# Kernel optimization log

Measured on AMD Instinct MI355X. Metric: run time of the kernel, lower is better.

Reference implementation:

```python
import jax, jax.numpy as jnp
import numpy as np
from jax.scipy.linalg import expm

N_QUBITS = 13
N_LAYERS = 4  # ceil(log2(13))


def _apply_2axes(T, M, a0, a1):
    """Apply 4x4 matrix M to the pair of 2-dim axes (a0, a1) of tensor T."""
    nd = T.ndim
    T = jnp.moveaxis(T, (a0, a1), (nd - 2, nd - 1))
    s = T.shape
    T = (T.reshape(s[:-2] + (4,)) @ M.T).reshape(s)
    return jnp.moveaxis(T, (nd - 2, nd - 1), (a0, a1))


def _conv_pairs(n):
    pairs = [(2 * i, 2 * i + 1) for i in range(n // 2)]
    if n > 2:
        pairs += [(2 * i + 1, (2 * i + 2) % n) for i in range(n // 2)]
    return pairs


def _conv_state(psi, U, n):
    # psi: [B] + [2]*n pure state
    for q0, q1 in _conv_pairs(n):
        psi = _apply_2axes(psi, U, 1 + q0, 1 + q1)
    return psi


def _conv_dm(rho, U, n):
    # rho: [B] + [2]*n (rows) + [2]*n (cols); apply U on rows, U* on cols
    Uc = U.conj()
    for q0, q1 in _conv_pairs(n):
        rho = _apply_2axes(rho, U, 1 + q0, 1 + q1)
        rho = _apply_2axes(rho, Uc, 1 + n + q0, 1 + n + q1)
    return rho


def _pool_dm(rho, n):
    # measure-and-discard qubits 0..n//2-1 (with index shifting these are the
    # original even-indexed qubits); averaging over outcomes == partial trace.
    measured = [2 * i for i in range(n // 2)]
    cur = n
    for q in reversed(measured):  # descending so lower indices stay valid
        rho = jnp.trace(rho, axis1=1 + q, axis2=1 + cur + q)
        cur -= 1
    return rho, cur


def setup_inputs() -> dict:
    key = jax.random.key(0)
    k1, k2, k3, k4 = jax.random.split(key, 4)
    B, D = 2, 2 ** N_QUBITS
    return {
        "psi_real": jax.random.normal(k1, (B, D), dtype=jnp.float32),
        "psi_imag": jax.random.normal(k2, (B, D), dtype=jnp.float32),
        "H_real": jax.random.normal(k3, (N_LAYERS, 4, 4), dtype=jnp.float32),
        "H_imag": jax.random.normal(k4, (N_LAYERS, 4, 4), dtype=jnp.float32),
    }


def reference(psi_real, psi_imag, H_real, H_imag):
    B = psi_real.shape[0]
    n = N_QUBITS
    psi = (psi_real + 1j * psi_imag).astype(jnp.complex64)
    psi = psi / jnp.linalg.norm(psi, axis=1, keepdims=True)
    H = (H_real + 1j * H_imag).astype(jnp.complex64)
    # anti-hermitian generator -> unitary gate per layer
    Us = [expm(H[i] - H[i].conj().T) for i in range(N_LAYERS)]

    # layer 0: conv on pure state, then convert to density matrix, then pool
    psi = psi.reshape((B,) + (2,) * n)
    psi = _conv_state(psi, Us[0], n)
    flat = psi.reshape(B, -1)
    rho = (flat[:, :, None] * flat[:, None, :].conj()).reshape((B,) + (2,) * (2 * n))
    rho, n = _pool_dm(rho, n)

    for i in range(1, N_LAYERS):
        rho = _conv_dm(rho, Us[i], n)
        rho, n = _pool_dm(rho, n)

    # n == 1 here: measure qubit 0, return P(outcome 0)
    rho = rho.reshape(B, 2, 2)
    return rho[:, 0, 0].real
```

## Files before the change

kernel.cpp:

```cpp
#include <hip/hip_runtime.h>


#define NT 512
#define DIM 8192

__device__ __forceinline__ float2 cadd(float2 a, float2 b) {
    return make_float2(a.x + b.x, a.y + b.y);
}
__device__ __forceinline__ float2 cmac(float2 acc, float2 a, float2 b) {
    acc.x = fmaf(a.x, b.x, fmaf(-a.y, b.y, acc.x));
    acc.y = fmaf(a.x, b.y, fmaf(a.y, b.x, acc.y));
    return acc;
}
__device__ __forceinline__ float2 shflc(float2 v, int src) {
    return make_float2(__shfl(v.x, src, 64), __shfl(v.y, src, 64));
}
__device__ __forceinline__ float2 cmac2(float2 acc, float2 u, float2 us, float2 a) {
    acc.x = fmaf(a.x, u.x, acc.x);
    acc.y = fmaf(a.x, u.y, acc.y);
    acc.x = fmaf(a.y, us.x, acc.x);
    acc.y = fmaf(a.y, us.y, acc.y);
    return acc;
}

__device__ float2 expm_entry(const float* __restrict__ Hr,
                             const float* __restrict__ Hi) {
    const int lane = threadIdx.x & 63;
    const int m = lane >> 4, e = lane & 15, r = e >> 2, c = e & 3;
    const int base = lane & 48;

    float are = Hr[m * 16 + r * 4 + c] - Hr[m * 16 + c * 4 + r];
    float aim = Hi[m * 16 + r * 4 + c] + Hi[m * 16 + c * 4 + r];

    float v = fabsf(are) + fabsf(aim);
    v += __shfl_xor(v, 1, 64);
    v += __shfl_xor(v, 2, 64);
    v = fmaxf(v, __shfl_xor(v, 4, 64));
    v = fmaxf(v, __shfl_xor(v, 8, 64));
    v = fmaxf(v, __shfl_xor(v, 16, 64));
    v = fmaxf(v, __shfl_xor(v, 32, 64));

    int s = 0;
    while (v > 0.25f && s < 30) { v *= 0.5f; s++; }
    const float scale = ldexpf(1.0f, -s);

    float2 X = make_float2(are * scale, aim * scale);
    float2 E = X;
    if (r == c) E.x += 1.0f;
    float2 T = X;
    for (int k = 2; k <= 10; k++) {
        float2 acc = make_float2(0.f, 0.f);
        #pragma unroll
        for (int kk = 0; kk < 4; kk++) {
            float2 t = shflc(T, base + r * 4 + kk);
            float2 x = shflc(X, base + kk * 4 + c);
            acc = cmac(acc, t, x);
        }
        const float inv = 1.0f / (float)k;
        T = make_float2(acc.x * inv, acc.y * inv);
        E = cadd(E, T);
    }
    for (int i = 0; i < s; i++) {
        float2 acc = make_float2(0.f, 0.f);
        #pragma unroll
        for (int kk = 0; kk < 4; kk++) {
            float2 a = shflc(E, base + r * 4 + kk);
            float2 bb = shflc(E, base + kk * 4 + c);
            acc = cmac(acc, a, bb);
        }
        E = acc;
    }
    return E;
}

__device__ __forceinline__ void loadU(float2 E, int L, float2* u, float2* us) {
    #pragma unroll
    for (int e = 0; e < 16; e++) {
        u[e] = shflc(E, (L << 4) | e);
        us[e] = make_float2(-u[e].y, u[e].x);
    }
}

__device__ __forceinline__ int swz(int e) {
    return e ^ ((e >> 4) & 15) ^ ((e >> 8) & 3);
}

template<int MASK>
__device__ __forceinline__ int deposit(int t) {
    int r = 0;
    #pragma unroll
    for (int bpos = 0; bpos < 13; bpos++) {
        if (MASK & (1 << bpos)) { r |= (t & 1) << bpos; t >>= 1; }
    }
    return r;
}

template<int B3, int B2, int B1, int B0>
__device__ __forceinline__ int eaddr(int base, int i) {
    return base | (((i >> 3) & 1) << B3) | (((i >> 2) & 1) << B2)
                | (((i >> 1) & 1) << B1) | ((i & 1) << B0);
}

template<int B3, int B2, int B1, int B0, int MASK>
__device__ __forceinline__ void phase_read(float2* v, const float2* psi, int t) {
    const int base = deposit<MASK>(t);
    #pragma unroll
    for (int i = 0; i < 16; i++) v[i] = psi[swz(eaddr<B3, B2, B1, B0>(base, i))];
}
template<int B3, int B2, int B1, int B0, int MASK>
__device__ __forceinline__ void phase_write(const float2* v, float2* psi, int t) {
    const int base = deposit<MASK>(t);
    #pragma unroll
    for (int i = 0; i < 16; i++) psi[swz(eaddr<B3, B2, B1, B0>(base, i))] = v[i];
}

template<int KA, int KB>
__device__ __forceinline__ void apply_gate(float2* v, const float2* u, const float2* us) {
    const int MA = 1 << KA, MB = 1 << KB;
    #pragma unroll
    for (int i = 0; i < 16; i++) {
        if (i & (MA | MB)) continue;
        float2 a0 = v[i], a1 = v[i | MB], a2 = v[i | MA], a3 = v[i | MA | MB];
        float2 n0 = make_float2(0.f, 0.f);
        n0 = cmac2(n0, u[0], us[0], a0);  n0 = cmac2(n0, u[1], us[1], a1);
        n0 = cmac2(n0, u[2], us[2], a2);  n0 = cmac2(n0, u[3], us[3], a3);
        float2 n1 = make_float2(0.f, 0.f);
        n1 = cmac2(n1, u[4], us[4], a0);  n1 = cmac2(n1, u[5], us[5], a1);
        n1 = cmac2(n1, u[6], us[6], a2);  n1 = cmac2(n1, u[7], us[7], a3);
        float2 n2 = make_float2(0.f, 0.f);
        n2 = cmac2(n2, u[8], us[8], a0);  n2 = cmac2(n2, u[9], us[9], a1);
        n2 = cmac2(n2, u[10], us[10], a2); n2 = cmac2(n2, u[11], us[11], a3);
        float2 n3 = make_float2(0.f, 0.f);
        n3 = cmac2(n3, u[12], us[12], a0); n3 = cmac2(n3, u[13], us[13], a1);
        n3 = cmac2(n3, u[14], us[14], a2); n3 = cmac2(n3, u[15], us[15], a3);
        v[i] = n0; v[i | MB] = n1; v[i | MA] = n2; v[i | MA | MB] = n3;
    }
}

__global__ __launch_bounds__(NT) void qcnn_kernel(
    const float* __restrict__ pr, const float* __restrict__ pi,
    const float* __restrict__ Hr, const float* __restrict__ Hi,
    float* __restrict__ out) {
    __shared__ float2 psi[DIM];
    const int tid = threadIdx.x;
    const int b = blockIdx.x;

    const float* prb = pr + b * DIM;
    const float* pib = pi + b * DIM;
    float re[16], im[16];
    #pragma unroll
    for (int i = 0; i < 16; i++) {
        re[i] = prb[tid | (i << 9)];
        im[i] = pib[tid | (i << 9)];
    }

    float2 E = expm_entry(Hr, Hi);

    float2 v[16];
    float norm2p = 0.f;
    #pragma unroll
    for (int i = 0; i < 16; i++) {
        v[i] = make_float2(re[i], im[i]);
        norm2p = fmaf(re[i], re[i], fmaf(im[i], im[i], norm2p));
    }

    float2 u[16], us[16];
    loadU(E, 0, u, us);

    apply_gate<3, 2>(v, u, us);
    apply_gate<1, 0>(v, u, us);
    apply_gate<2, 1>(v, u, us);
    phase_write<12, 11, 10, 9, 0x01FF>(v, psi, tid);
    __syncthreads();

    phase_read<8, 7, 6, 5, 0x1E1F>(v, psi, tid);
    apply_gate<3, 2>(v, u, us);
    apply_gate<1, 0>(v, u, us);
    apply_gate<2, 1>(v, u, us);
    phase_write<8, 7, 6, 5, 0x1E1F>(v, psi, tid);
    __syncthreads();

    phase_read<3, 2, 1, 0, 0x1FF0>(v, psi, tid);
    apply_gate<2, 1>(v, u, us);
    apply_gate<1, 0>(v, u, us);
    phase_write<3, 2, 1, 0, 0x1FF0>(v, psi, tid);
    __syncthreads();

    phase_read<5, 4, 3, 2, 0x1FC3>(v, psi, tid);
    apply_gate<2, 1>(v, u, us);
    apply_gate<3, 2>(v, u, us);
    apply_gate<1, 0>(v, u, us);
    phase_write<5, 4, 3, 2, 0x1FC3>(v, psi, tid);
    __syncthreads();

    phase_read<11, 9, 8, 7, 0x147F>(v, psi, tid);
    apply_gate<2, 1>(v, u, us);
    loadU(E, 1, u, us);
    apply_gate<3, 2>(v, u, us);
    phase_write<11, 9, 8, 7, 0x147F>(v, psi, tid);
    __syncthreads();

    phase_read<7, 5, 3, 1, 0x1F55>(v, psi, tid);
    apply_gate<3, 2>(v, u, us);
    apply_gate<1, 0>(v, u, us);
    apply_gate<2, 1>(v, u, us);
    phase_write<7, 5, 3, 1, 0x1F55>(v, psi, tid);
    __syncthreads();

    phase_read<9, 7, 1, 0, 0x1D7C>(v, psi, tid);
    apply_gate<3, 2>(v, u, us);
    apply_gate<1, 0>(v, u, us);
    loadU(E, 2, u, us);
    apply_gate<1, 0>(v, u, us);
    phase_write<9, 7, 1, 0, 0x1D7C>(v, psi, tid);
    __syncthreads();

    phase_read<9, 5, 1, 0, 0x1DDC>(v, psi, tid);
    apply_gate<3, 2>(v, u, us);
    apply_gate<2, 1>(v, u, us);
    apply_gate<0, 3>(v, u, us);
    loadU(E, 3, u, us);
    apply_gate<2, 0>(v, u, us);

    float s0 = 0.f;
    #pragma unroll
    for (int i = 0; i < 16; i += 2) {
        s0 = fmaf(v[i].x, v[i].x, fmaf(v[i].y, v[i].y, s0));
    }

    #pragma unroll
    for (int off = 1; off < 64; off <<= 1) {
        s0 += __shfl_xor(s0, off, 64);
        norm2p += __shfl_xor(norm2p, off, 64);
    }
    __syncthreads();
    if ((tid & 63) == 0) psi[tid >> 6] = make_float2(s0, norm2p);
    __syncthreads();
    if (tid == 0) {
        float S = 0.f, Nrm = 0.f;
        #pragma unroll
        for (int w = 0; w < NT / 64; w++) { S += psi[w].x; Nrm += psi[w].y; }
        out[b] = S / Nrm;
    }
}

extern "C" void kernel_launch(void* const* d_in, const int* in_sizes, int n_in,
                              void* d_out, int out_size, void* d_ws, size_t ws_size,
                              hipStream_t stream) {
    const float* pr = (const float*)d_in[0];
    const float* pi = (const float*)d_in[1];
    const float* Hr = (const float*)d_in[2];
    const float* Hi = (const float*)d_in[3];
    float* out = (float*)d_out;
    qcnn_kernel<<<dim3(out_size), dim3(NT), 0, stream>>>(pr, pi, Hr, Hi, out);
}
```

Measured before the change: 81.50 us.

## Use 32 amplitudes per thread with 5-qubit phases to cut LDS round trips

Halves the block to 256 threads so each thread holds 32 amplitudes covering 5 qubits, and redesigns the gate schedule so fewer shared-memory exchange phases and barriers are needed (six instead of seven). The complex multiply-accumulate is rewritten on 2-wide vector types to encourage packed FP32 FMA instructions, and the LDS swizzle is changed to match the new access patterns. The cost is higher register pressure (64 floats of state plus the gate matrices) and fewer threads for latency hiding.

```diff
diff --git a/kernel.cpp b/kernel.cpp
--- a/kernel.cpp
+++ b/kernel.cpp
@@ -1,13 +1,15 @@
 #include <hip/hip_runtime.h>
 
 
-#define NT 512
+#define NT 256
 #define DIM 8192
 
-__device__ __forceinline__ float2 cadd(float2 a, float2 b) {
+typedef float v2f __attribute__((ext_vector_type(2)));
+
+__device__ __forceinline__ float2 cadds(float2 a, float2 b) {
     return make_float2(a.x + b.x, a.y + b.y);
 }
-__device__ __forceinline__ float2 cmac(float2 acc, float2 a, float2 b) {
+__device__ __forceinline__ float2 cmacs(float2 acc, float2 a, float2 b) {
     acc.x = fmaf(a.x, b.x, fmaf(-a.y, b.y, acc.x));
     acc.y = fmaf(a.x, b.y, fmaf(a.y, b.x, acc.y));
     return acc;
@@ -15,22 +17,20 @@
 __device__ __forceinline__ float2 shflc(float2 v, int src) {
     return make_float2(__shfl(v.x, src, 64), __shfl(v.y, src, 64));
 }
-__device__ __forceinline__ float2 cmac2(float2 acc, float2 u, float2 us, float2 a) {
-    acc.x = fmaf(a.x, u.x, acc.x);
-    acc.y = fmaf(a.x, u.y, acc.y);
-    acc.x = fmaf(a.y, us.x, acc.x);
-    acc.y = fmaf(a.y, us.y, acc.y);
+
+__device__ __forceinline__ v2f cma(v2f acc, v2f u, v2f us, v2f a) {
+#pragma clang fp contract(fast)
+    v2f ax = __builtin_shufflevector(a, a, 0, 0);
+    v2f ay = __builtin_shufflevector(a, a, 1, 1);
+    acc = ax * u + acc;
+    acc = ay * us + acc;
     return acc;
 }
 
-__device__ float2 expm_entry(const float* __restrict__ Hr,
-                             const float* __restrict__ Hi) {
+__device__ float2 expm_compute(float are, float aim) {
     const int lane = threadIdx.x & 63;
-    const int m = lane >> 4, e = lane & 15, r = e >> 2, c = e & 3;
+    const int e = lane & 15, r = e >> 2, c = e & 3;
     const int base = lane & 48;
-
-    float are = Hr[m * 16 + r * 4 + c] - Hr[m * 16 + c * 4 + r];
-    float aim = Hi[m * 16 + r * 4 + c] + Hi[m * 16 + c * 4 + r];
 
     float v = fabsf(are) + fabsf(aim);
     v += __shfl_xor(v, 1, 64);
@@ -54,11 +54,11 @@
         for (int kk = 0; kk < 4; kk++) {
             float2 t = shflc(T, base + r * 4 + kk);
             float2 x = shflc(X, base + kk * 4 + c);
-            acc = cmac(acc, t, x);
+            acc = cmacs(acc, t, x);
         }
         const float inv = 1.0f / (float)k;
         T = make_float2(acc.x * inv, acc.y * inv);
-        E = cadd(E, T);
+        E = cadds(E, T);
     }
     for (int i = 0; i < s; i++) {
         float2 acc = make_float2(0.f, 0.f);
@@ -66,157 +66,152 @@
         for (int kk = 0; kk < 4; kk++) {
             float2 a = shflc(E, base + r * 4 + kk);
             float2 bb = shflc(E, base + kk * 4 + c);
-            acc = cmac(acc, a, bb);
+            acc = cmacs(acc, a, bb);
         }
         E = acc;
     }
     return E;
 }
 
-__device__ __forceinline__ void loadU(float2 E, int L, float2* u, float2* us) {
-    #pragma unroll
-    for (int e = 0; e < 16; e++) {
-        u[e] = shflc(E, (L << 4) | e);
-        us[e] = make_float2(-u[e].y, u[e].x);
+__device__ __forceinline__ void loadU(float2 E, int L, v2f* u, v2f* us) {
+    #pragma unroll
+    for (int k = 0; k < 16; k++) {
+        float ur = __shfl(E.x, (L << 4) | k, 64);
+        float ui = __shfl(E.y, (L << 4) | k, 64);
+        u[k] = (v2f){ur, ui};
+        us[k] = (v2f){-ui, ur};
     }
 }
 
 __device__ __forceinline__ int swz(int e) {
-    return e ^ ((e >> 4) & 15) ^ ((e >> 8) & 3);
+    return e ^ ((e >> 3) & 14) ^ ((e >> 7) & 15) ^ ((e >> 10) & 14);
 }
 
 template<int MASK>
 __device__ __forceinline__ int deposit(int t) {
     int r = 0;
     #pragma unroll
-    for (int bpos = 0; bpos < 13; bpos++) {
-        if (MASK & (1 << bpos)) { r |= (t & 1) << bpos; t >>= 1; }
+    for (int p = 0; p < 13; p++) {
+        if (MASK & (1 << p)) { r |= (t & 1) << p; t >>= 1; }
     }
     return r;
 }
 
-template<int B3, int B2, int B1, int B0>
-__device__ __forceinline__ int eaddr(int base, int i) {
-    return base | (((i >> 3) & 1) << B3) | (((i >> 2) & 1) << B2)
-                | (((i >> 1) & 1) << B1) | ((i & 1) << B0);
-}
-
-template<int B3, int B2, int B1, int B0, int MASK>
-__device__ __forceinline__ void phase_read(float2* v, const float2* psi, int t) {
+template<int B4, int B3, int B2, int B1, int B0>
+__device__ __forceinline__ int eaddr5(int base, int i) {
+    return base | (((i >> 4) & 1) << B4) | (((i >> 3) & 1) << B3)
+                | (((i >> 2) & 1) << B2) | (((i >> 1) & 1) << B1)
+                | ((i & 1) << B0);
+}
+
+template<int B4, int B3, int B2, int B1, int B0, int MASK>
+__device__ __forceinline__ void phase_read(v2f* v, const v2f* psi, int t) {
     const int base = deposit<MASK>(t);
     #pragma unroll
-    for (int i = 0; i < 16; i++) v[i] = psi[swz(eaddr<B3, B2, B1, B0>(base, i))];
-}
-template<int B3, int B2, int B1, int B0, int MASK>
-__device__ __forceinline__ void phase_write(const float2* v, float2* psi, int t) {
+    for (int i = 0; i < 32; i++) v[i] = psi[swz(eaddr5<B4, B3, B2, B1, B0>(base, i))];
+}
+template<int B4, int B3, int B2, int B1, int B0, int MASK>
+__device__ __forceinline__ void phase_write(const v2f* v, v2f* psi, int t) {
     const int base = deposit<MASK>(t);
     #pragma unroll
-    for (int i = 0; i < 16; i++) psi[swz(eaddr<B3, B2, B1, B0>(base, i))] = v[i];
+    for (int i = 0; i < 32; i++) psi[swz(eaddr5<B4, B3, B2, B1, B0>(base, i))] = v[i];
 }
 
 template<int KA, int KB>
-__device__ __forceinline__ void apply_gate(float2* v, const float2* u, const float2* us) {
+__device__ __forceinline__ void apply_gate(v2f* v, const v2f* u, const v2f* us) {
     const int MA = 1 << KA, MB = 1 << KB;
     #pragma unroll
-    for (int i = 0; i < 16; i++) {
+    for (int i = 0; i < 32; i++) {
         if (i & (MA | MB)) continue;
-        float2 a0 = v[i], a1 = v[i | MB], a2 = v[i | MA], a3 = v[i | MA | MB];
-        float2 n0 = make_float2(0.f, 0.f);
-        n0 = cmac2(n0, u[0], us[0], a0);  n0 = cmac2(n0, u[1], us[1], a1);
-        n0 = cmac2(n0, u[2], us[2], a2);  n0 = cmac2(n0, u[3], us[3], a3);
-        float2 n1 = make_float2(0.f, 0.f);
-        n1 = cmac2(n1, u[4], us[4], a0);  n1 = cmac2(n1, u[5], us[5], a1);
-        n1 = cmac2(n1, u[6], us[6], a2);  n1 = cmac2(n1, u[7], us[7], a3);
-        float2 n2 = make_float2(0.f, 0.f);
-        n2 = cmac2(n2, u[8], us[8], a0);  n2 = cmac2(n2, u[9], us[9], a1);
-        n2 = cmac2(n2, u[10], us[10], a2); n2 = cmac2(n2, u[11], us[11], a3);
-        float2 n3 = make_float2(0.f, 0.f);
-        n3 = cmac2(n3, u[12], us[12], a0); n3 = cmac2(n3, u[13], us[13], a1);
-        n3 = cmac2(n3, u[14], us[14], a2); n3 = cmac2(n3, u[15], us[15], a3);
+        v2f a0 = v[i], a1 = v[i | MB], a2 = v[i | MA], a3 = v[i | MA | MB];
+        v2f z = {0.f, 0.f};
+        v2f n0 = cma(cma(cma(cma(z, u[0], us[0], a0), u[1], us[1], a1),
+                         u[2], us[2], a2), u[3], us[3], a3);
+        v2f n1 = cma(cma(cma(cma(z, u[4], us[4], a0), u[5], us[5], a1),
+                         u[6], us[6], a2), u[7], us[7], a3);
+        v2f n2 = cma(cma(cma(cma(z, u[8], us[8], a0), u[9], us[9], a1),
+                         u[10], us[10], a2), u[11], us[11], a3);
+        v2f n3 = cma(cma(cma(cma(z, u[12], us[12], a0), u[13], us[13], a1),
+                         u[14], us[14], a2), u[15], us[15], a3);
         v[i] = n0; v[i | MB] = n1; v[i | MA] = n2; v[i | MA | MB] = n3;
     }
 }
 
-__global__ __launch_bounds__(NT) void qcnn_kernel(
+__global__ __launch_bounds__(NT, 1) void qcnn_kernel(
     const float* __restrict__ pr, const float* __restrict__ pi,
     const float* __restrict__ Hr, const float* __restrict__ Hi,
     float* __restrict__ out) {
-    __shared__ float2 psi[DIM];
-    const int tid = threadIdx.x;
+    __shared__ v2f psi[DIM];
+    const int t = threadIdx.x;
     const int b = blockIdx.x;
+    const int lane = t & 63;
+    const int m = lane >> 4, ee = lane & 15, r = ee >> 2, c = ee & 3;
+
+    float hra = Hr[m * 16 + r * 4 + c], hrb = Hr[m * 16 + c * 4 + r];
+    float hia = Hi[m * 16 + r * 4 + c], hib = Hi[m * 16 + c * 4 + r];
 
     const float* prb = pr + b * DIM;
     const float* pib = pi + b * DIM;
-    float re[16], im[16];
-    #pragma unroll
-    for (int i = 0; i < 16; i++) {
-        re[i] = prb[tid | (i << 9)];
-        im[i] = pib[tid | (i << 9)];
-    }
-
-    float2 E = expm_entry(Hr, Hi);
-
-    float2 v[16];
-    float norm2p = 0.f;
-    #pragma unroll
-    for (int i = 0; i < 16; i++) {
-        v[i] = make_float2(re[i], im[i]);
-        norm2p = fmaf(re[i], re[i], fmaf(im[i], im[i], norm2p));
-    }
-
-    float2 u[16], us[16];
+    v2f v[32];
+    #pragma unroll
+    for (int i = 0; i < 32; i++)
+        v[i] = (v2f){prb[t | (i << 8)], pib[t | (i << 8)]};
+
+    float2 E = expm_compute(hra - hrb, hia + hib);
+
+    float norm2 = 0.f;
+    #pragma unroll
+    for (int i = 0; i < 32; i++)
+        norm2 = fmaf(v[i].x, v[i].x, fmaf(v[i].y, v[i].y, norm2));
+
+    v2f u[16], us[16];
     loadU(E, 0, u, us);
 
-    apply_gate<3, 2>(v, u, us);
-    apply_gate<1, 0>(v, u, us);
-    apply_gate<2, 1>(v, u, us);
-    phase_write<12, 11, 10, 9, 0x01FF>(v, psi, tid);
-    __syncthreads();
-
-    phase_read<8, 7, 6, 5, 0x1E1F>(v, psi, tid);
-    apply_gate<3, 2>(v, u, us);
-    apply_gate<1, 0>(v, u, us);
-    apply_gate<2, 1>(v, u, us);
-    phase_write<8, 7, 6, 5, 0x1E1F>(v, psi, tid);
-    __syncthreads();
-
-    phase_read<3, 2, 1, 0, 0x1FF0>(v, psi, tid);
-    apply_gate<2, 1>(v, u, us);
-    apply_gate<1, 0>(v, u, us);
-    phase_write<3, 2, 1, 0, 0x1FF0>(v, psi, tid);
-    __syncthreads();
-
-    phase_read<5, 4, 3, 2, 0x1FC3>(v, psi, tid);
-    apply_gate<2, 1>(v, u, us);
-    apply_gate<3, 2>(v, u, us);
-    apply_gate<1, 0>(v, u, us);
-    phase_write<5, 4, 3, 2, 0x1FC3>(v, psi, tid);
-    __syncthreads();
-
-    phase_read<11, 9, 8, 7, 0x147F>(v, psi, tid);
-    apply_gate<2, 1>(v, u, us);
+    apply_gate<4, 3>(v, u, us);
+    apply_gate<2, 1>(v, u, us);
+    apply_gate<3, 2>(v, u, us);
+    phase_write<12, 11, 10, 9, 8, 0x00FF>(v, psi, t);
+    __syncthreads();
+
+    phase_read<8, 7, 6, 5, 4, 0x1E0F>(v, psi, t);
+    apply_gate<4, 3>(v, u, us);
+    apply_gate<2, 1>(v, u, us);
+    apply_gate<3, 2>(v, u, us);
+    phase_write<8, 7, 6, 5, 4, 0x1E0F>(v, psi, t);
+    __syncthreads();
+
+    phase_read<4, 3, 2, 1, 0, 0x1FE0>(v, psi, t);
+    apply_gate<4, 3>(v, u, us);
+    apply_gate<2, 1>(v, u, us);
+    apply_gate<3, 2>(v, u, us);
+    apply_gate<1, 0>(v, u, us);
     loadU(E, 1, u, us);
-    apply_gate<3, 2>(v, u, us);
-    phase_write<11, 9, 8, 7, 0x147F>(v, psi, tid);
-    __syncthreads();
-
-    phase_read<7, 5, 3, 1, 0x1F55>(v, psi, tid);
-    apply_gate<3, 2>(v, u, us);
-    apply_gate<1, 0>(v, u, us);
-    apply_gate<2, 1>(v, u, us);
-    phase_write<7, 5, 3, 1, 0x1F55>(v, psi, tid);
-    __syncthreads();
-
-    phase_read<9, 7, 1, 0, 0x1D7C>(v, psi, tid);
-    apply_gate<3, 2>(v, u, us);
+    apply_gate<3, 1>(v, u, us);
     apply_gate<1, 0>(v, u, us);
     loadU(E, 2, u, us);
     apply_gate<1, 0>(v, u, us);
-    phase_write<9, 7, 1, 0, 0x1D7C>(v, psi, tid);
-    __syncthreads();
-
-    phase_read<9, 5, 1, 0, 0x1DDC>(v, psi, tid);
-    apply_gate<3, 2>(v, u, us);
+    phase_write<4, 3, 2, 1, 0, 0x1FE0>(v, psi, t);
+    __syncthreads();
+
+    phase_read<9, 8, 7, 5, 4, 0x1C4F>(v, psi, t);
+    loadU(E, 0, u, us);
+    apply_gate<4, 3>(v, u, us);
+    apply_gate<1, 0>(v, u, us);
+    loadU(E, 1, u, us);
+    apply_gate<2, 1>(v, u, us);
+    phase_write<9, 8, 7, 5, 4, 0x1C4F>(v, psi, t);
+    __syncthreads();
+
+    phase_read<11, 9, 7, 5, 3, 0x1557>(v, psi, t);
+    apply_gate<4, 3>(v, u, us);
+    apply_gate<3, 2>(v, u, us);
+    apply_gate<1, 0>(v, u, us);
+    loadU(E, 2, u, us);
+    apply_gate<3, 1>(v, u, us);
+    phase_write<11, 9, 7, 5, 3, 0x1557>(v, psi, t);
+    __syncthreads();
+
+    phase_read<12, 9, 5, 1, 0, 0x0DDC>(v, psi, t);
     apply_gate<2, 1>(v, u, us);
     apply_gate<0, 3>(v, u, us);
     loadU(E, 3, u, us);
@@ -224,19 +219,18 @@
 
     float s0 = 0.f;
     #pragma unroll
-    for (int i = 0; i < 16; i += 2) {
+    for (int i = 0; i < 32; i += 2)
         s0 = fmaf(v[i].x, v[i].x, fmaf(v[i].y, v[i].y, s0));
-    }
 
     #pragma unroll
     for (int off = 1; off < 64; off <<= 1) {
         s0 += __shfl_xor(s0, off, 64);
-        norm2p += __shfl_xor(norm2p, off, 64);
-    }
-    __syncthreads();
-    if ((tid & 63) == 0) psi[tid >> 6] = make_float2(s0, norm2p);
-    __syncthreads();
-    if (tid == 0) {
+        norm2 += __shfl_xor(norm2, off, 64);
+    }
+    __syncthreads();
+    if (lane == 0) psi[t >> 6] = (v2f){s0, norm2};
+    __syncthreads();
+    if (t == 0) {
         float S = 0.f, Nrm = 0.f;
         #pragma unroll
         for (int w = 0; w < NT / 64; w++) { S += psi[w].x; Nrm += psi[w].y; }
```

Measured after the change: 82.47 us. No clear change (+1.2%).
